# Kernel optimization log

Hardware: AMD Instinct MI355X
Metric: run time of the kernel (lower is better)

Reference implementation:

```python
import jax, jax.numpy as jnp
import numpy as np
import math

L, N, E, H = 2048, 4, 1024, 16  # seq_len, batch, embed_dim, num_heads
HD = E // H                      # head_dim = 64


def setup_inputs() -> dict:
    key = jax.random.key(0)
    ks = jax.random.split(key, 7)
    s = 1.0 / math.sqrt(E)
    return {
        "query": jax.random.normal(ks[0], (L, N, E), jnp.float32),
        "key": jax.random.normal(ks[1], (L, N, E), jnp.float32),
        "value": jax.random.normal(ks[2], (L, N, E), jnp.float32),
        "in_proj_weight": jax.random.normal(ks[3], (3 * E, E), jnp.float32) * s,
        "in_proj_bias": jax.random.normal(ks[4], (3 * E,), jnp.float32) * 0.02,
        "out_proj_weight": jax.random.normal(ks[5], (E, E), jnp.float32) * s,
        "out_proj_bias": jax.random.normal(ks[6], (E,), jnp.float32) * 0.02,
    }


def reference(query, key, value, in_proj_weight, in_proj_bias,
              out_proj_weight, out_proj_bias):
    # --- packed in-projection (q is k is v path of _in_projection_packed) ---
    # F.linear(x, W, b) = x @ W.T + b, W packed as [Wq; Wk; Wv] along dim 0.
    wq, wk, wv = jnp.split(in_proj_weight, 3, axis=0)   # each (E, E)
    bq, bk, bv = jnp.split(in_proj_bias, 3, axis=0)     # each (E,)
    q = query @ wq.T + bq   # (L, N, E)
    k = key @ wk.T + bk
    v = value @ wv.T + bv

    # --- split heads: (L, N, E) -> (N*H, L, HD), matching torch reshape/transpose ---
    def to_heads(x):
        return x.reshape(L, N * H, HD).transpose(1, 0, 2)
    q, k, v = to_heads(q), to_heads(k), to_heads(v)

    # --- scaled dot-product attention (q scaled by 1/sqrt(head_dim)) ---
    q = q / math.sqrt(HD)
    attn = jnp.einsum('bte,bse->bts', q, k)             # (N*H, L, L)
    attn = jax.nn.softmax(attn, axis=-1)
    out = jnp.einsum('bts,bse->bte', attn, v)           # (N*H, L, HD)

    # --- merge heads back to (L, N, E) ---
    out = out.transpose(1, 0, 2).reshape(L, N, E)

    # --- out-projection ---
    out = out @ out_proj_weight.T + out_proj_bias       # (L, N, E)
    return out
```

## Files before the change

kernel.cpp:

```cpp
#include <hip/hip_runtime.h>

using f16 = _Float16;
typedef _Float16 h8 __attribute__((ext_vector_type(8)));
typedef _Float16 h4 __attribute__((ext_vector_type(4)));
typedef float f32x4 __attribute__((ext_vector_type(4)));
typedef float f32x16 __attribute__((ext_vector_type(16)));
typedef unsigned u32x4 __attribute__((ext_vector_type(4)));

constexpr int L_SEQ  = 2048;
constexpr int NBATCH = 4;
constexpr int EMB    = 1024;
constexpr int NHEAD  = 16;
constexpr int HDIM   = 64;
constexpr int BH     = NBATCH * NHEAD;
constexpr int MROWS  = L_SEQ * NBATCH;

#define QSCALE (0.125f * 1.44269504088896341f)

__device__ __forceinline__ void glds16(const void* g, void* l) {
  __builtin_amdgcn_global_load_lds(
      (const __attribute__((address_space(1))) void*)g,
      (__attribute__((address_space(3))) void*)l, 16, 0, 0);
}

__device__ __forceinline__ f32x16 MFMA32(h8 a, h8 b, f32x16 c) {
  return __builtin_amdgcn_mfma_f32_32x32x16_f16(a, b, c, 0, 0, 0);
}
__device__ __forceinline__ unsigned pkrtz(float x, float y) {
  auto t = __builtin_amdgcn_cvt_pkrtz(x, y);
  return __builtin_bit_cast(unsigned, t);
}
__device__ __forceinline__ h8 pack8(f32x4 a, f32x4 b) {
  u32x4 u = { pkrtz(a[0], a[1]), pkrtz(a[2], a[3]),
              pkrtz(b[0], b[1]), pkrtz(b[2], b[3]) };
  return __builtin_bit_cast(h8, u);
}

__global__ __launch_bounds__(256)
void convert_w_kernel(const float* __restrict__ w, const float* __restrict__ wo,
                      f16* __restrict__ wb, f16* __restrict__ wob) {
  const int NW  = 3 * EMB * EMB / 4;
  const int NWO = EMB * EMB / 4;
  const int total = NW + NWO;
  int i = blockIdx.x * blockDim.x + threadIdx.x;
  const int stride = gridDim.x * blockDim.x;
  for (; i < total; i += stride) {
    const float* s; f16* d; int j;
    if (i < NW) { s = w;  d = wb;  j = i;      }
    else        { s = wo; d = wob; j = i - NW; }
    float4 t = reinterpret_cast<const float4*>(s)[j];
    h4 o = { (f16)t.x, (f16)t.y, (f16)t.z, (f16)t.w };
    reinterpret_cast<h4*>(d)[j] = o;
  }
}

__global__ __launch_bounds__(256)
void gemm_qkv(const float* __restrict__ qin, const float* __restrict__ kin,
              const float* __restrict__ vin, const f16* __restrict__ Btbase,
              const float* __restrict__ biasbase, f16* __restrict__ Hbase)
{
  const int id = blockIdx.x;
  const int x   = id & 7;
  const int bnI = (id >> 3) & 7;
  const int bmG = x + 8 * (id >> 6);
  const int z   = bmG >> 6;
  const int bm  = (bmG & 63) * 128;
  const int bn  = bnI * 128;

  const float* A = (z == 0) ? qin : (z == 1) ? kin : vin;
  const f16* Bt = Btbase + (size_t)z * EMB * EMB;
  const float* bias = biasbase + (size_t)z * EMB;

  const int t = threadIdx.x;
  const int w = t >> 6, lane = t & 63;
  const int wr = w >> 1, wc = w & 1;
  const int l16 = lane & 15, g = lane >> 4;

  __shared__ f16 As[2][128][32];
  __shared__ f16 Bs[2][128][32];

  f32x4 acc[4][4] = {};

  const int sr0 = lane >> 2;
  const int sl  = lane & 3;
  const float* gA = &A[(size_t)(bm + w*32 + sr0) * EMB + sl*8];
  const int wslot = 8 * (sl ^ ((sr0 >> 1) & 3));
  f16* lA0 = &As[0][w*32 + sr0][wslot];
  f16* lA0b = &As[0][w*32 + 16 + sr0][wslot];
  const int asStride = 128 * 32;

  const int sr  = lane >> 2;
  const int sc8 = 8 * ((lane & 3) ^ ((lane >> 3) & 3));
  const f16* gB = &Bt[(size_t)(bn + w*32 + sr) * EMB + sc8];

  f32x4 ra0, ra1, rb0, rb1;
  f32x4 sa0, sa1, sb0, sb1;

  ra0 = *(const f32x4*)(gA);
  ra1 = *(const f32x4*)(gA + 4);
  rb0 = *(const f32x4*)(gA + (size_t)16*EMB);
  rb1 = *(const f32x4*)(gA + (size_t)16*EMB + 4);
  *(h8*)lA0  = pack8(ra0, ra1);
  *(h8*)lA0b = pack8(rb0, rb1);
  glds16(gB, &Bs[0][w*32][0]);
  glds16(gB + (size_t)16*EMB, &Bs[0][w*32 + 16][0]);
  sa0 = *(const f32x4*)(gA + 32);
  sa1 = *(const f32x4*)(gA + 36);
  sb0 = *(const f32x4*)(gA + (size_t)16*EMB + 32);
  sb1 = *(const f32x4*)(gA + (size_t)16*EMB + 36);
  glds16(gB + 32, &Bs[1][w*32][0]);
  glds16(gB + (size_t)16*EMB + 32, &Bs[1][w*32 + 16][0]);
  __syncthreads();

  const int fswz = (g ^ ((l16 >> 1) & 3)) * 8;

#pragma unroll 2
  for (int i = 0; i < 32; ++i) {
    const int cur = i & 1;
    if (i < 30) {
      const int k0 = (i + 2) * 32;
      ra0 = *(const f32x4*)(gA + k0);
      ra1 = *(const f32x4*)(gA + k0 + 4);
      rb0 = *(const f32x4*)(gA + (size_t)16*EMB + k0);
      rb1 = *(const f32x4*)(gA + (size_t)16*EMB + k0 + 4);
    }
    if (i < 31) {
      const int k0 = (i + 1) * 32;
      glds16(gB + k0, &Bs[cur ^ 1][w*32][0]);
      glds16(gB + (size_t)16*EMB + k0, &Bs[cur ^ 1][w*32 + 16][0]);
    }

    h8 af[4], bfr[4];
#pragma unroll
    for (int m = 0; m < 4; ++m) af[m]  = *(const h8*)&As[cur][wr*64 + m*16 + l16][fswz];
#pragma unroll
    for (int n = 0; n < 4; ++n) bfr[n] = *(const h8*)&Bs[cur][wc*64 + n*16 + l16][fswz];
    __builtin_amdgcn_s_setprio(1);
#pragma unroll
    for (int m = 0; m < 4; ++m)
#pragma unroll
      for (int n = 0; n < 4; ++n)
        acc[m][n] = __builtin_amdgcn_mfma_f32_16x16x32_f16(af[m], bfr[n], acc[m][n], 0, 0, 0);
    __builtin_amdgcn_s_setprio(0);

    if (i < 31) {
      f16* d0 = lA0  + (cur ^ 1) * asStride;
      f16* d1 = lA0b + (cur ^ 1) * asStride;
      *(h8*)d0 = pack8(sa0, sa1);
      *(h8*)d1 = pack8(sb0, sb1);
      sa0 = ra0; sa1 = ra1; sb0 = rb0; sb1 = rb1;
    }
    __syncthreads();
  }

#pragma unroll
  for (int m = 0; m < 4; ++m) {
#pragma unroll
    for (int n = 0; n < 4; ++n) {
      const int col = bn + wc*64 + n*16 + l16;
      const float bv = bias[col];
#pragma unroll
      for (int r = 0; r < 4; ++r) {
        const int row = bm + wr*64 + m*16 + g*4 + r;
        float v = acc[m][n][r] + bv;
        if (z == 0) v *= QSCALE;
        const int l = row >> 2, nn = row & 3;
        const int h = col >> 6, hd = col & 63;
        Hbase[(((size_t)z * BH + nn * NHEAD + h) * L_SEQ + l) * HDIM + hd] = (f16)v;
      }
    }
  }
}

__global__ __launch_bounds__(256)
void gemm_out(const f16* __restrict__ A, const f16* __restrict__ Bt,
              const float* __restrict__ bias, float* __restrict__ Fout)
{
  const int id = blockIdx.x;
  const int x   = id & 7;
  const int bnI = (id >> 3) & 7;
  const int bmG = x + 8 * (id >> 6);
  const int bm  = bmG * 128;
  const int bn  = bnI * 128;

  const int t = threadIdx.x;
  const int w = t >> 6, lane = t & 63;
  const int wr = w >> 1, wc = w & 1;
  const int l16 = lane & 15, g = lane >> 4;

  __shared__ f16 As[2][128][32];
  __shared__ f16 Bs[2][128][32];

  f32x4 acc[4][4] = {};

  const int sr  = lane >> 2;
  const int sc8 = 8 * ((lane & 3) ^ ((lane >> 3) & 3));
  const f16* gA = &A [(size_t)(bm + w*32 + sr) * EMB + sc8];
  const f16* gB = &Bt[(size_t)(bn + w*32 + sr) * EMB + sc8];

  glds16(gA, &As[0][w*32][0]);
  glds16(gA + (size_t)16*EMB, &As[0][w*32 + 16][0]);
  glds16(gB, &Bs[0][w*32][0]);
  glds16(gB + (size_t)16*EMB, &Bs[0][w*32 + 16][0]);
  __syncthreads();

  const int fswz = (g ^ ((l16 >> 1) & 3)) * 8;

#pragma unroll 1
  for (int i = 0; i < 32; ++i) {
    const int cur = i & 1;
    if (i < 31) {
      const int k0 = (i + 1) * 32;
      glds16(gA + k0, &As[cur ^ 1][w*32][0]);
      glds16(gA + (size_t)16*EMB + k0, &As[cur ^ 1][w*32 + 16][0]);
      glds16(gB + k0, &Bs[cur ^ 1][w*32][0]);
      glds16(gB + (size_t)16*EMB + k0, &Bs[cur ^ 1][w*32 + 16][0]);
    }

    h8 af[4], bfr[4];
#pragma unroll
    for (int m = 0; m < 4; ++m) af[m]  = *(const h8*)&As[cur][wr*64 + m*16 + l16][fswz];
#pragma unroll
    for (int n = 0; n < 4; ++n) bfr[n] = *(const h8*)&Bs[cur][wc*64 + n*16 + l16][fswz];
    __builtin_amdgcn_s_setprio(1);
#pragma unroll
    for (int m = 0; m < 4; ++m)
#pragma unroll
      for (int n = 0; n < 4; ++n)
        acc[m][n] = __builtin_amdgcn_mfma_f32_16x16x32_f16(af[m], bfr[n], acc[m][n], 0, 0, 0);
    __builtin_amdgcn_s_setprio(0);
    __syncthreads();
  }

#pragma unroll
  for (int m = 0; m < 4; ++m) {
#pragma unroll
    for (int n = 0; n < 4; ++n) {
      const int col = bn + wc*64 + n*16 + l16;
      const float bv = bias[col];
#pragma unroll
      for (int r = 0; r < 4; ++r) {
        const int row = bm + wr*64 + m*16 + g*4 + r;
        Fout[(size_t)row * EMB + col] = acc[m][n][r] + bv;
      }
    }
  }
}

__global__ __launch_bounds__(256)
void vtrans_kernel(const f16* __restrict__ V, f16* __restrict__ Vt) {
  const int b = blockIdx.y;
  const int t = threadIdx.x;
  const int d = t & 63;
  const int l0 = (blockIdx.x * 4 + (t >> 6)) * 8;
  const f16* Vb = V  + (size_t)b * L_SEQ * HDIM;
  f16* Vtb      = Vt + (size_t)b * L_SEQ * HDIM;
  h8 v;
#pragma unroll
  for (int i = 0; i < 8; ++i) v[i] = Vb[(size_t)(l0 + i) * HDIM + d];
  *(h8*)&Vtb[(size_t)d * L_SEQ + l0] = v;
}

__device__ __forceinline__ void expack(const f32x16& acc, float (&ps)[4],
                                       h8& paA, h8& paB) {
#pragma unroll
  for (int half = 0; half < 2; ++half) {
    float p0 = __builtin_amdgcn_exp2f(acc[half*8+0]);
    float p1 = __builtin_amdgcn_exp2f(acc[half*8+1]);
    float p2 = __builtin_amdgcn_exp2f(acc[half*8+2]);
    float p3 = __builtin_amdgcn_exp2f(acc[half*8+3]);
    float p4 = __builtin_amdgcn_exp2f(acc[half*8+4]);
    float p5 = __builtin_amdgcn_exp2f(acc[half*8+5]);
    float p6 = __builtin_amdgcn_exp2f(acc[half*8+6]);
    float p7 = __builtin_amdgcn_exp2f(acc[half*8+7]);
    ps[0] += p0 + p4;
    ps[1] += p1 + p5;
    ps[2] += p2 + p6;
    ps[3] += p3 + p7;
    unsigned A = pkrtz(p0, p1);
    unsigned C = pkrtz(p2, p3);
    unsigned B = pkrtz(p4, p5);
    unsigned D = pkrtz(p6, p7);
    asm("v_permlane32_swap_b32 %0, %1" : "+v"(A), "+v"(B));
    asm("v_permlane32_swap_b32 %0, %1" : "+v"(C), "+v"(D));
    u32x4 wv = { A, C, B, D };
    h8 r = __builtin_bit_cast(h8, wv);
    if (half == 0) paA = r; else paB = r;
  }
}

__device__ __forceinline__ void attn12_step(
    const f16* __restrict__ Kc, const f16* __restrict__ Vc,
    const h8 (&qf0)[4], const h8 (&qf1)[4],
    f32x16 (&o0)[2], f32x16 (&o1)[2],
    float (&ps0)[4], float (&ps1)[4],
    int l31, int hi)
{
  const int swz = (l31 & 7) << 3;

  h8 pa0[4], pa1[4];
#pragma unroll
  for (int kt = 0; kt < 2; ++kt) {
    h8 kf[4];
#pragma unroll
    for (int s = 0; s < 4; ++s)
      kf[s] = *(const h8*)&Kc[(kt*32 + l31)*64 + ((s*16 + hi*8) ^ swz)];

    f32x16 acc0 = {};
    f32x16 acc1 = {};
    __builtin_amdgcn_s_setprio(1);
#pragma unroll
    for (int s = 0; s < 4; ++s) {
      acc0 = MFMA32(kf[s], qf0[s], acc0);
      acc1 = MFMA32(kf[s], qf1[s], acc1);
    }
    __builtin_amdgcn_s_setprio(0);

    expack(acc0, ps0, pa0[kt*2], pa0[kt*2+1]);
    expack(acc1, ps1, pa1[kt*2], pa1[kt*2+1]);
  }

#pragma unroll
  for (int s2 = 0; s2 < 4; ++s2) {
    h8 vf0 = *(const h8*)&Vc[(0*32 + l31)*64 + ((s2*16 + hi*8) ^ swz)];
    h8 vf1 = *(const h8*)&Vc[(1*32 + l31)*64 + ((s2*16 + hi*8) ^ swz)];
    __builtin_amdgcn_s_setprio(1);
    o0[0] = MFMA32(pa0[s2], vf0, o0[0]);
    o0[1] = MFMA32(pa0[s2], vf1, o0[1]);
    o1[0] = MFMA32(pa1[s2], vf0, o1[0]);
    o1[1] = MFMA32(pa1[s2], vf1, o1[1]);
    __builtin_amdgcn_s_setprio(0);
  }
}

__global__ __launch_bounds__(256, 2)
void attn12_kernel(const f16* __restrict__ Qh, const f16* __restrict__ Kh,
                   const f16* __restrict__ Vt, f16* __restrict__ AO)
{
  const int id = blockIdx.x;
  const int b    = (id & 7) | ((id >> 6) << 3);
  const int qblk = (id >> 3) & 7;

  const int t = threadIdx.x;
  const int w = t >> 6, lane = t & 63;
  const int l31 = lane & 31, hi = lane >> 5;

  const f16* Qb = Qh + (size_t)b * L_SEQ * HDIM;
  const f16* Kb = Kh + (size_t)b * L_SEQ * HDIM;
  const f16* Vb = Vt + (size_t)b * (size_t)HDIM * L_SEQ;

  __shared__ f16 Ks[2][64*64];
  __shared__ f16 Vs[2][64*64];

  const int q0 = qblk * 256 + w * 32;

  h8 qf0[4], qf1[4];
#pragma unroll
  for (int s = 0; s < 4; ++s) {
    qf0[s] = *(const h8*)&Qb[(size_t)(q0 + l31) * HDIM + s*16 + hi*8];
    qf1[s] = *(const h8*)&Qb[(size_t)(q0 + 128 + l31) * HDIM + s*16 + hi*8];
  }

  const int srow = lane >> 3;
  const int scol = 8 * ((lane & 7) ^ srow);
  const int r0   = w*16 + srow;
  const f16* gK0 = Kb + (size_t)(r0    ) * HDIM + scol;
  const f16* gK1 = Kb + (size_t)(r0 + 8) * HDIM + scol;
  const f16* gV0 = Vb + (size_t)(r0    ) * L_SEQ + scol;
  const f16* gV1 = Vb + (size_t)(r0 + 8) * L_SEQ + scol;
  const int ldsw = w * 1024;

  f32x16 o0[2] = {};
  f32x16 o1[2] = {};
  float ps0[4] = { 0.f, 0.f, 0.f, 0.f };
  float ps1[4] = { 0.f, 0.f, 0.f, 0.f };

  glds16(gK0, &Ks[0][ldsw]);
  glds16(gK1, &Ks[0][ldsw + 512]);
  glds16(gV0, &Vs[0][ldsw]);
  glds16(gV1, &Vs[0][ldsw + 512]);
  __syncthreads();

#pragma unroll 1
  for (int j0 = 0; j0 < L_SEQ; j0 += 128) {
    {
      const int jn = (j0 + 64) & (L_SEQ - 1);
      glds16(gK0 + (size_t)jn * HDIM, &Ks[1][ldsw]);
      glds16(gK1 + (size_t)jn * HDIM, &Ks[1][ldsw + 512]);
      glds16(gV0 + jn, &Vs[1][ldsw]);
      glds16(gV1 + jn, &Vs[1][ldsw + 512]);
      attn12_step(&Ks[0][0], &Vs[0][0], qf0, qf1, o0, o1, ps0, ps1, l31, hi);
      __syncthreads();
    }
    {
      const int jn = (j0 + 128) & (L_SEQ - 1);
      glds16(gK0 + (size_t)jn * HDIM, &Ks[0][ldsw]);
      glds16(gK1 + (size_t)jn * HDIM, &Ks[0][ldsw + 512]);
      glds16(gV0 + jn, &Vs[0][ldsw]);
      glds16(gV1 + jn, &Vs[0][ldsw + 512]);
      attn12_step(&Ks[1][0], &Vs[1][0], qf0, qf1, o0, o1, ps0, ps1, l31, hi);
      __syncthreads();
    }
  }

  const int nn = b >> 4, h = b & 15;
  float ssum0 = (ps0[0] + ps0[1]) + (ps0[2] + ps0[3]);
  ssum0 += __shfl_xor(ssum0, 32);
  const float inv0 = 1.0f / ssum0;
  float ssum1 = (ps1[0] + ps1[1]) + (ps1[2] + ps1[3]);
  ssum1 += __shfl_xor(ssum1, 32);
  const float inv1 = 1.0f / ssum1;

#pragma unroll
  for (int r = 0; r < 16; ++r) {
    const int qrow = (r & 3) + 8 * (r >> 2) + 4 * hi;
    {
      const float iv = __shfl(inv0, qrow);
      const int lr = q0 + qrow;
#pragma unroll
      for (int dt = 0; dt < 2; ++dt)
        AO[((size_t)lr * NBATCH + nn) * EMB + h*HDIM + dt*32 + l31] =
            (f16)(o0[dt][r] * iv);
    }
    {
      const float iv = __shfl(inv1, qrow);
      const int lr = q0 + 128 + qrow;
#pragma unroll
      for (int dt = 0; dt < 2; ++dt)
        AO[((size_t)lr * NBATCH + nn) * EMB + h*HDIM + dt*32 + l31] =
            (f16)(o1[dt][r] * iv);
    }
  }
}

extern "C" void kernel_launch(void* const* d_in, const int* in_sizes, int n_in,
                              void* d_out, int out_size, void* d_ws, size_t ws_size,
                              hipStream_t stream) {
  const float* query = (const float*)d_in[0];
  const float* key   = (const float*)d_in[1];
  const float* value = (const float*)d_in[2];
  const float* in_w  = (const float*)d_in[3];
  const float* in_b  = (const float*)d_in[4];
  const float* out_w = (const float*)d_in[5];
  const float* out_b = (const float*)d_in[6];
  float* out = (float*)d_out;

  char* ws = (char*)d_ws;
  size_t offH  = 0;
  size_t offX  = offH  + (size_t)3 * BH * L_SEQ * HDIM * 2;
  size_t offW  = offX  + (size_t)3 * MROWS * EMB * 2;
  size_t offWo = offW  + (size_t)3 * EMB * EMB * 2;
  size_t offAO = offWo + (size_t)EMB * EMB * 2;
  f16* Hbase = (f16*)(ws + offH);
  f16* Xb    = (f16*)(ws + offX);
  f16* Wb    = (f16*)(ws + offW);
  f16* Wob   = (f16*)(ws + offWo);
  f16* AOb   = (f16*)(ws + offAO);
  f16* Vtb   = Xb;

  hipLaunchKernelGGL(convert_w_kernel, dim3(1024), dim3(256), 0, stream,
                     in_w, out_w, Wb, Wob);

  hipLaunchKernelGGL(gemm_qkv, dim3(1536), dim3(256), 0, stream,
                     query, key, value, Wb, in_b, Hbase);

  f16* Vh = Hbase + (size_t)2 * BH * L_SEQ * HDIM;
  hipLaunchKernelGGL(vtrans_kernel, dim3(L_SEQ/32, BH), dim3(256), 0, stream, Vh, Vtb);

  hipLaunchKernelGGL(attn12_kernel, dim3(512), dim3(256), 0, stream,
                     Hbase,
                     Hbase + (size_t)BH * L_SEQ * HDIM,
                     Vtb, AOb);

  hipLaunchKernelGGL(gemm_out, dim3(512), dim3(256), 0, stream,
                     AOb, Wob, out_b, out);
}
```

Measured before the change: 207.8 us.

## Fuse fp32-to-fp16 weight conversion into QKV and output projection GEMM loads

Removes the separate weight conversion kernel. The QKV and output-projection GEMMs now read fp32 weights directly, convert them in registers and store them as fp16 into swizzled LDS, with register double-buffering like the existing A path. This saves one kernel launch and the write-then-read of 8 MB of fp16 weights. In exchange, every GEMM block reads fp32 weights, which doubles weight bytes per tile load and adds register pressure and conversion work inside the main loop.

```diff
diff --git a/kernel.cpp b/kernel.cpp
--- a/kernel.cpp
+++ b/kernel.cpp
@@ -37,26 +37,8 @@
 }
 
 __global__ __launch_bounds__(256)
-void convert_w_kernel(const float* __restrict__ w, const float* __restrict__ wo,
-                      f16* __restrict__ wb, f16* __restrict__ wob) {
-  const int NW  = 3 * EMB * EMB / 4;
-  const int NWO = EMB * EMB / 4;
-  const int total = NW + NWO;
-  int i = blockIdx.x * blockDim.x + threadIdx.x;
-  const int stride = gridDim.x * blockDim.x;
-  for (; i < total; i += stride) {
-    const float* s; f16* d; int j;
-    if (i < NW) { s = w;  d = wb;  j = i;      }
-    else        { s = wo; d = wob; j = i - NW; }
-    float4 t = reinterpret_cast<const float4*>(s)[j];
-    h4 o = { (f16)t.x, (f16)t.y, (f16)t.z, (f16)t.w };
-    reinterpret_cast<h4*>(d)[j] = o;
-  }
-}
-
-__global__ __launch_bounds__(256)
 void gemm_qkv(const float* __restrict__ qin, const float* __restrict__ kin,
-              const float* __restrict__ vin, const f16* __restrict__ Btbase,
+              const float* __restrict__ vin, const float* __restrict__ Wbase,
               const float* __restrict__ biasbase, f16* __restrict__ Hbase)
 {
   const int id = blockIdx.x;
@@ -68,7 +50,7 @@
   const int bn  = bnI * 128;
 
   const float* A = (z == 0) ? qin : (z == 1) ? kin : vin;
-  const f16* Bt = Btbase + (size_t)z * EMB * EMB;
+  const float* Bt = Wbase + (size_t)z * EMB * EMB;
   const float* bias = biasbase + (size_t)z * EMB;
 
   const int t = threadIdx.x;
@@ -83,33 +65,40 @@
 
   const int sr0 = lane >> 2;
   const int sl  = lane & 3;
-  const float* gA = &A[(size_t)(bm + w*32 + sr0) * EMB + sl*8];
   const int wslot = 8 * (sl ^ ((sr0 >> 1) & 3));
-  f16* lA0 = &As[0][w*32 + sr0][wslot];
+  const float* gA = &A [(size_t)(bm + w*32 + sr0) * EMB + sl*8];
+  const float* gBf = &Bt[(size_t)(bn + w*32 + sr0) * EMB + sl*8];
+  f16* lA0  = &As[0][w*32 + sr0][wslot];
   f16* lA0b = &As[0][w*32 + 16 + sr0][wslot];
+  f16* lB0  = &Bs[0][w*32 + sr0][wslot];
+  f16* lB0b = &Bs[0][w*32 + 16 + sr0][wslot];
   const int asStride = 128 * 32;
-
-  const int sr  = lane >> 2;
-  const int sc8 = 8 * ((lane & 3) ^ ((lane >> 3) & 3));
-  const f16* gB = &Bt[(size_t)(bn + w*32 + sr) * EMB + sc8];
 
   f32x4 ra0, ra1, rb0, rb1;
   f32x4 sa0, sa1, sb0, sb1;
+  f32x4 rc0, rc1, rd0, rd1;
+  f32x4 sc0, sc1, sd0, sd1;
 
   ra0 = *(const f32x4*)(gA);
   ra1 = *(const f32x4*)(gA + 4);
   rb0 = *(const f32x4*)(gA + (size_t)16*EMB);
   rb1 = *(const f32x4*)(gA + (size_t)16*EMB + 4);
+  rc0 = *(const f32x4*)(gBf);
+  rc1 = *(const f32x4*)(gBf + 4);
+  rd0 = *(const f32x4*)(gBf + (size_t)16*EMB);
+  rd1 = *(const f32x4*)(gBf + (size_t)16*EMB + 4);
   *(h8*)lA0  = pack8(ra0, ra1);
   *(h8*)lA0b = pack8(rb0, rb1);
-  glds16(gB, &Bs[0][w*32][0]);
-  glds16(gB + (size_t)16*EMB, &Bs[0][w*32 + 16][0]);
+  *(h8*)lB0  = pack8(rc0, rc1);
+  *(h8*)lB0b = pack8(rd0, rd1);
   sa0 = *(const f32x4*)(gA + 32);
   sa1 = *(const f32x4*)(gA + 36);
   sb0 = *(const f32x4*)(gA + (size_t)16*EMB + 32);
   sb1 = *(const f32x4*)(gA + (size_t)16*EMB + 36);
-  glds16(gB + 32, &Bs[1][w*32][0]);
-  glds16(gB + (size_t)16*EMB + 32, &Bs[1][w*32 + 16][0]);
+  sc0 = *(const f32x4*)(gBf + 32);
+  sc1 = *(const f32x4*)(gBf + 36);
+  sd0 = *(const f32x4*)(gBf + (size_t)16*EMB + 32);
+  sd1 = *(const f32x4*)(gBf + (size_t)16*EMB + 36);
   __syncthreads();
 
   const int fswz = (g ^ ((l16 >> 1) & 3)) * 8;
@@ -123,11 +112,10 @@
       ra1 = *(const f32x4*)(gA + k0 + 4);
       rb0 = *(const f32x4*)(gA + (size_t)16*EMB + k0);
       rb1 = *(const f32x4*)(gA + (size_t)16*EMB + k0 + 4);
-    }
-    if (i < 31) {
-      const int k0 = (i + 1) * 32;
-      glds16(gB + k0, &Bs[cur ^ 1][w*32][0]);
-      glds16(gB + (size_t)16*EMB + k0, &Bs[cur ^ 1][w*32 + 16][0]);
+      rc0 = *(const f32x4*)(gBf + k0);
+      rc1 = *(const f32x4*)(gBf + k0 + 4);
+      rd0 = *(const f32x4*)(gBf + (size_t)16*EMB + k0);
+      rd1 = *(const f32x4*)(gBf + (size_t)16*EMB + k0 + 4);
     }
 
     h8 af[4], bfr[4];
@@ -146,9 +134,14 @@
     if (i < 31) {
       f16* d0 = lA0  + (cur ^ 1) * asStride;
       f16* d1 = lA0b + (cur ^ 1) * asStride;
+      f16* d2 = lB0  + (cur ^ 1) * asStride;
+      f16* d3 = lB0b + (cur ^ 1) * asStride;
       *(h8*)d0 = pack8(sa0, sa1);
       *(h8*)d1 = pack8(sb0, sb1);
+      *(h8*)d2 = pack8(sc0, sc1);
+      *(h8*)d3 = pack8(sd0, sd1);
       sa0 = ra0; sa1 = ra1; sb0 = rb0; sb1 = rb1;
+      sc0 = rc0; sc1 = rc1; sd0 = rd0; sd1 = rd1;
     }
     __syncthreads();
   }
@@ -173,7 +166,7 @@
 }
 
 __global__ __launch_bounds__(256)
-void gemm_out(const f16* __restrict__ A, const f16* __restrict__ Bt,
+void gemm_out(const f16* __restrict__ A, const float* __restrict__ Wo,
               const float* __restrict__ bias, float* __restrict__ Fout)
 {
   const int id = blockIdx.x;
@@ -195,26 +188,49 @@
 
   const int sr  = lane >> 2;
   const int sc8 = 8 * ((lane & 3) ^ ((lane >> 3) & 3));
-  const f16* gA = &A [(size_t)(bm + w*32 + sr) * EMB + sc8];
-  const f16* gB = &Bt[(size_t)(bn + w*32 + sr) * EMB + sc8];
+  const f16* gA = &A[(size_t)(bm + w*32 + sr) * EMB + sc8];
+
+  const int sr0 = lane >> 2;
+  const int sl  = lane & 3;
+  const int wslot = 8 * (sl ^ ((sr0 >> 1) & 3));
+  const float* gBf = &Wo[(size_t)(bn + w*32 + sr0) * EMB + sl*8];
+  f16* lB0  = &Bs[0][w*32 + sr0][wslot];
+  f16* lB0b = &Bs[0][w*32 + 16 + sr0][wslot];
+  const int bsStride = 128 * 32;
+
+  f32x4 rc0, rc1, rd0, rd1;
+  f32x4 sc0, sc1, sd0, sd1;
 
   glds16(gA, &As[0][w*32][0]);
   glds16(gA + (size_t)16*EMB, &As[0][w*32 + 16][0]);
-  glds16(gB, &Bs[0][w*32][0]);
-  glds16(gB + (size_t)16*EMB, &Bs[0][w*32 + 16][0]);
+  rc0 = *(const f32x4*)(gBf);
+  rc1 = *(const f32x4*)(gBf + 4);
+  rd0 = *(const f32x4*)(gBf + (size_t)16*EMB);
+  rd1 = *(const f32x4*)(gBf + (size_t)16*EMB + 4);
+  *(h8*)lB0  = pack8(rc0, rc1);
+  *(h8*)lB0b = pack8(rd0, rd1);
+  sc0 = *(const f32x4*)(gBf + 32);
+  sc1 = *(const f32x4*)(gBf + 36);
+  sd0 = *(const f32x4*)(gBf + (size_t)16*EMB + 32);
+  sd1 = *(const f32x4*)(gBf + (size_t)16*EMB + 36);
   __syncthreads();
 
   const int fswz = (g ^ ((l16 >> 1) & 3)) * 8;
 
-#pragma unroll 1
+#pragma unroll 2
   for (int i = 0; i < 32; ++i) {
     const int cur = i & 1;
     if (i < 31) {
       const int k0 = (i + 1) * 32;
       glds16(gA + k0, &As[cur ^ 1][w*32][0]);
       glds16(gA + (size_t)16*EMB + k0, &As[cur ^ 1][w*32 + 16][0]);
-      glds16(gB + k0, &Bs[cur ^ 1][w*32][0]);
-      glds16(gB + (size_t)16*EMB + k0, &Bs[cur ^ 1][w*32 + 16][0]);
+    }
+    if (i < 30) {
+      const int k0 = (i + 2) * 32;
+      rc0 = *(const f32x4*)(gBf + k0);
+      rc1 = *(const f32x4*)(gBf + k0 + 4);
+      rd0 = *(const f32x4*)(gBf + (size_t)16*EMB + k0);
+      rd1 = *(const f32x4*)(gBf + (size_t)16*EMB + k0 + 4);
     }
 
     h8 af[4], bfr[4];
@@ -229,6 +245,14 @@
       for (int n = 0; n < 4; ++n)
         acc[m][n] = __builtin_amdgcn_mfma_f32_16x16x32_f16(af[m], bfr[n], acc[m][n], 0, 0, 0);
     __builtin_amdgcn_s_setprio(0);
+
+    if (i < 31) {
+      f16* d2 = lB0  + (cur ^ 1) * bsStride;
+      f16* d3 = lB0b + (cur ^ 1) * bsStride;
+      *(h8*)d2 = pack8(sc0, sc1);
+      *(h8*)d3 = pack8(sd0, sd1);
+      sc0 = rc0; sc1 = rc1; sd0 = rd0; sd1 = rd1;
+    }
     __syncthreads();
   }
 
@@ -448,21 +472,14 @@
   char* ws = (char*)d_ws;
   size_t offH  = 0;
   size_t offX  = offH  + (size_t)3 * BH * L_SEQ * HDIM * 2;
-  size_t offW  = offX  + (size_t)3 * MROWS * EMB * 2;
-  size_t offWo = offW  + (size_t)3 * EMB * EMB * 2;
-  size_t offAO = offWo + (size_t)EMB * EMB * 2;
+  size_t offAO = offX  + (size_t)3 * MROWS * EMB * 2;
   f16* Hbase = (f16*)(ws + offH);
   f16* Xb    = (f16*)(ws + offX);
-  f16* Wb    = (f16*)(ws + offW);
-  f16* Wob   = (f16*)(ws + offWo);
   f16* AOb   = (f16*)(ws + offAO);
   f16* Vtb   = Xb;
 
-  hipLaunchKernelGGL(convert_w_kernel, dim3(1024), dim3(256), 0, stream,
-                     in_w, out_w, Wb, Wob);
-
   hipLaunchKernelGGL(gemm_qkv, dim3(1536), dim3(256), 0, stream,
-                     query, key, value, Wb, in_b, Hbase);
+                     query, key, value, in_w, in_b, Hbase);
 
   f16* Vh = Hbase + (size_t)2 * BH * L_SEQ * HDIM;
   hipLaunchKernelGGL(vtrans_kernel, dim3(L_SEQ/32, BH), dim3(256), 0, stream, Vh, Vtb);
@@ -473,5 +490,5 @@
                      Vtb, AOb);
 
   hipLaunchKernelGGL(gemm_out, dim3(512), dim3(256), 0, stream,
-                     AOb, Wob, out_b, out);
-}
+                     AOb, out_w, out_b, out);
+}
```

Result: slower. 230.5 us (+10.9%).
